# Kernel optimization log

Measured on AMD Instinct MI355X. Metric: run time of the kernel, lower is better.

The kernel has to match this reference:

```python
import jax, jax.numpy as jnp
import numpy as np

BN_EPS = 1e-5


def _l2norm(v, eps=1e-12):
    return v / (jnp.linalg.norm(v) + eps)


def _sn_weight(W, u):
    # torch spectral_norm, n_power_iterations=1; u, v detached, grad flows via W
    v = _l2norm(W.T @ u)
    u_new = _l2norm(W @ v)
    u_new = jax.lax.stop_gradient(u_new)
    v = jax.lax.stop_gradient(v)
    sigma = u_new @ (W @ v)
    return W / sigma


def setup_inputs() -> dict:
    key = jax.random.key(0)
    ks = jax.random.split(key, 8)
    N, E, nfeat, nhid = 65536, 1048576, 64, 128
    x = jax.random.normal(ks[0], (N, nfeat), dtype=jnp.float32)
    edge_index = jax.random.randint(ks[1], (2, E), 0, N, dtype=jnp.int64)
    s1 = 1.0 / np.sqrt(nfeat)
    s2 = 1.0 / np.sqrt(nhid)
    W1 = jax.random.uniform(ks[2], (nhid, nfeat), jnp.float32, -s1, s1)
    b1 = jax.random.uniform(ks[3], (nhid,), jnp.float32, -s1, s1)
    u1 = jax.random.normal(ks[4], (nhid,), dtype=jnp.float32)
    gamma = jnp.ones((nhid,), jnp.float32)
    beta = jnp.zeros((nhid,), jnp.float32)
    W2 = jax.random.uniform(ks[5], (nhid, nhid), jnp.float32, -s2, s2)
    b2 = jax.random.uniform(ks[6], (nhid,), jnp.float32, -s2, s2)
    u2 = jax.random.normal(ks[7], (nhid,), dtype=jnp.float32)
    return {"x": x, "edge_index": edge_index, "W1": W1, "b1": b1, "u1": u1,
            "gamma": gamma, "beta": beta, "W2": W2, "b2": b2, "u2": u2}


def reference(x, edge_index, W1, b1, u1, gamma, beta, W2, b2, u2):
    N = x.shape[0]
    src, dst = edge_index[0], edge_index[1]
    # GIN neighbor sum aggregation: agg[i] = sum_{(j->i)} x[j]
    agg = jax.ops.segment_sum(x[src], dst, num_segments=N)
    h = x + agg  # (1 + eps) * x + agg, eps = 0
    # MLP: SN-Linear -> ReLU -> BatchNorm1d (training stats) -> SN-Linear
    h = h @ _sn_weight(W1, u1).T + b1
    h = jax.nn.relu(h)
    mean = jnp.mean(h, axis=0)
    var = jnp.var(h, axis=0)  # biased, as torch BN uses for normalization
    h = (h - mean) * jax.lax.rsqrt(var + BN_EPS) * gamma + beta
    out = h @ _sn_weight(W2, u2).T + b2
    return out
```

## Files before the change

kernel.cpp:

```cpp
#include <hip/hip_runtime.h>


#define BN_EPS 1e-5f
#define NB   512
#define CAP  2816

typedef float f4 __attribute__((ext_vector_type(4)));
typedef short bf8 __attribute__((ext_vector_type(8)));

__device__ inline short f2bf(float f) {
    unsigned u = __float_as_uint(f);
    u = u + 0x7fffu + ((u >> 16) & 1u);
    return (short)(u >> 16);
}
__device__ inline float bf2f(unsigned short u) {
    return __uint_as_float((unsigned)u << 16);
}
__device__ inline unsigned pk2(float a, float b) {
    return (unsigned)(unsigned short)f2bf(a) |
           ((unsigned)(unsigned short)f2bf(b) << 16);
}

__global__ __launch_bounds__(512) void k1_bin(const int* __restrict__ ei, int E,
                                              int* __restrict__ gcount,
                                              unsigned* __restrict__ pairs,
                                              const float* __restrict__ x,
                                              unsigned* __restrict__ xbf2,
                                              const float* __restrict__ W1,
                                              short* __restrict__ w1bf,
                                              const float* __restrict__ u1,
                                              const float* __restrict__ W2,
                                              const float* __restrict__ u2,
                                              float* __restrict__ sinv) {
    __shared__ int hist[512];
    __shared__ int sbase[512];
    __shared__ int cur[512];
    __shared__ int gofs[512];
    __shared__ unsigned stage[4096];
    int t = threadIdx.x;
    int bid = blockIdx.x;

    if (bid < 256) {
        hist[t] = 0;
        __syncthreads();

        const uint4* s4 = (const uint4*)ei + bid * 1024;
        const uint4* d4 = (const uint4*)(ei + E) + bid * 1024;
        unsigned pk[8];
#pragma unroll
        for (int i = 0; i < 2; i++) {
            int idx = i * 512 + t;
            uint4 sv = s4[idx];
            uint4 dv = d4[idx];
            pk[i * 4 + 0] = ((dv.x >> 7) << 23) | (sv.x << 7) | (dv.x & 127u);
            pk[i * 4 + 1] = ((dv.y >> 7) << 23) | (sv.y << 7) | (dv.y & 127u);
            pk[i * 4 + 2] = ((dv.z >> 7) << 23) | (sv.z << 7) | (dv.z & 127u);
            pk[i * 4 + 3] = ((dv.w >> 7) << 23) | (sv.w << 7) | (dv.w & 127u);
            atomicAdd(&hist[dv.x >> 7], 1);
            atomicAdd(&hist[dv.y >> 7], 1);
            atomicAdd(&hist[dv.z >> 7], 1);
            atomicAdd(&hist[dv.w >> 7], 1);
        }
        __syncthreads();

        int cntb = hist[t];
        for (int o = 1; o < 512; o <<= 1) {
            int v = (t >= o) ? hist[t - o] : 0;
            __syncthreads();
            hist[t] += v;
            __syncthreads();
        }
        int excl = hist[t] - cntb;
        sbase[t] = excl;
        cur[t] = excl;
        __syncthreads();

#pragma unroll
        for (int i = 0; i < 8; i++) {
            int p = atomicAdd(&cur[pk[i] >> 23], 1);
            stage[p] = pk[i];
        }
        __syncthreads();

        gofs[t] = atomicAdd(&gcount[t], cntb);
        __syncthreads();

#pragma unroll
        for (int i = 0; i < 8; i++) {
            int p = i * 512 + t;
            unsigned v = stage[p];
            int b = (int)(v >> 23);
            int li = p - sbase[b];
            pairs[(size_t)b * CAP + gofs[b] + li] = v & 0x7FFFFFu;
        }
    } else if (bid < 512) {
        int cb = bid - 256;
        const float4* xp = (const float4*)x;
#pragma unroll
        for (int k = 0; k < 4; k++) {
            int i = cb * 2048 + k * 512 + t;
            float4 a = xp[2 * i], b = xp[2 * i + 1];
            uint4 o = {pk2(a.x, a.y), pk2(a.z, a.w), pk2(b.x, b.y), pk2(b.z, b.w)};
            ((uint4*)xbf2)[i] = o;
        }
    } else {
#pragma unroll
        for (int k = 0; k < 2; k++) {
            int idx = k * 512 + t;
            const float4* wp = (const float4*)W1;
            float4 a = wp[2 * idx], b = wp[2 * idx + 1];
            uint4 o = {pk2(a.x, a.y), pk2(a.z, a.w), pk2(b.x, b.y), pk2(b.z, b.w)};
            ((uint4*)w1bf)[idx] = o;
        }
        float* red = (float*)stage;
        float* v   = (float*)hist;
        float* sq  = (float*)sbase;

        {
            int j = t & 63, q = t >> 6;
            float s = 0.f;
            for (int i = q * 16; i < q * 16 + 16; i++) s += W1[i * 64 + j] * u1[i];
            red[t] = s;
        }
        __syncthreads();
        if (t < 64) {
            float vj = 0.f;
#pragma unroll
            for (int g = 0; g < 8; g++) vj += red[g * 64 + t];
            v[t] = vj; sq[t] = vj * vj;
        }
        __syncthreads();
        for (int s2 = 32; s2 > 0; s2 >>= 1) {
            if (t < s2) sq[t] += sq[t + s2];
            __syncthreads();
        }
        if (t < 64) v[t] = v[t] / (sqrtf(sq[0]) + 1e-12f);
        __syncthreads();
        {
            int r = t >> 2, h = t & 3;
            const float4* wr = (const float4*)(W1 + r * 64 + h * 16);
            const float4* vv = (const float4*)v + h * 4;
            float s = 0.f;
#pragma unroll
            for (int k = 0; k < 4; k++) {
                float4 a = wr[k]; float4 b = vv[k];
                s += a.x * b.x + a.y * b.y + a.z * b.z + a.w * b.w;
            }
            red[t] = s;
        }
        __syncthreads();
        if (t < 128) {
            float tr = (red[4 * t] + red[4 * t + 1]) + (red[4 * t + 2] + red[4 * t + 3]);
            sq[t] = tr * tr;
        }
        __syncthreads();
        for (int s2 = 64; s2 > 0; s2 >>= 1) {
            if (t < s2) sq[t] += sq[t + s2];
            __syncthreads();
        }
        if (t == 0) { float nt2 = sq[0]; sinv[0] = (sqrtf(nt2) + 1e-12f) / nt2; }
        __syncthreads();

        {
            int j = t & 127, q = t >> 7;
            float s = 0.f;
            for (int i = q * 32; i < q * 32 + 32; i++) s += W2[i * 128 + j] * u2[i];
            red[t] = s;
        }
        __syncthreads();
        if (t < 128) {
            float vj = (red[t] + red[128 + t]) + (red[256 + t] + red[384 + t]);
            v[t] = vj; sq[t] = vj * vj;
        }
        __syncthreads();
        for (int s2 = 64; s2 > 0; s2 >>= 1) {
            if (t < s2) sq[t] += sq[t + s2];
            __syncthreads();
        }
        if (t < 128) v[t] = v[t] / (sqrtf(sq[0]) + 1e-12f);
        __syncthreads();
        {
            int r = t >> 2, h = t & 3;
            const float4* wr = (const float4*)(W2 + r * 128 + h * 32);
            const float4* vv = (const float4*)v + h * 8;
            float s = 0.f;
#pragma unroll
            for (int k = 0; k < 8; k++) {
                float4 a = wr[k]; float4 b = vv[k];
                s += a.x * b.x + a.y * b.y + a.z * b.z + a.w * b.w;
            }
            red[t] = s;
        }
        __syncthreads();
        if (t < 128) {
            float tr = (red[4 * t] + red[4 * t + 1]) + (red[4 * t + 2] + red[4 * t + 3]);
            sq[t] = tr * tr;
        }
        __syncthreads();
        for (int s2 = 64; s2 > 0; s2 >>= 1) {
            if (t < s2) sq[t] += sq[t + s2];
            __syncthreads();
        }
        if (t == 0) { float nt2 = sq[0]; sinv[1] = (sqrtf(nt2) + 1e-12f) / nt2; }
    }
}

__global__ __launch_bounds__(512) void k2_agg_gemm1(
        const unsigned* __restrict__ pairs,
        const int* __restrict__ gcount,
        const unsigned* __restrict__ xbf2,
        const short* __restrict__ w1bf,
        const float* __restrict__ b1,
        const float* __restrict__ sinv,
        char* __restrict__ outbase,
        float* __restrict__ bnacc) {
    __shared__ short u[16384];
    __shared__ unsigned short sorted[CAP];
    __shared__ int hist[128];
    __shared__ int offs[128];
    __shared__ int cur[128];
    __shared__ float red1[1024], red2[1024];
    int t = threadIdx.x;
    int b = blockIdx.x;
    int cnt = gcount[b];

    unsigned* ep = (unsigned*)u;
    {
        const uint4* gp4 = (const uint4*)(pairs + (size_t)b * CAP);
        int cnt4 = (cnt + 3) >> 2;
        for (int j = t; j < cnt4; j += 512) ((uint4*)ep)[j] = gp4[j];
    }
    if (t < 128) hist[t] = 0;
    __syncthreads();
    for (int j = t; j < cnt; j += 512) atomicAdd(&hist[ep[j] & 127u], 1);
    __syncthreads();
    int cntb = (t < 128) ? hist[t] : 0;
    for (int o = 1; o < 128; o <<= 1) {
        int v = (t < 128 && t >= o) ? hist[t - o] : 0;
        __syncthreads();
        if (t < 128) hist[t] += v;
        __syncthreads();
    }
    if (t < 128) { offs[t] = hist[t] - cntb; cur[t] = hist[t] - cntb; }
    __syncthreads();
    for (int j = t; j < cnt; j += 512) {
        unsigned v = ep[j];
        int p = atomicAdd(&cur[v & 127u], 1);
        sorted[p] = (unsigned short)(v >> 7);
    }
    __syncthreads();

    int w = t >> 6;
    int lane = t & 63;
    int h = lane >> 5;
    int l = lane & 31;
    float hr0[16], hr1[16];

#pragma unroll
    for (int ni = 0; ni < 16; ni++) {
        int n = w * 16 + ni;
        int g = b * 128 + n;
        int beg = offs[n], end = hist[n];
        float a0 = 0.f, a1 = 0.f, b0 = 0.f, b1r = 0.f;
        float c0 = 0.f, c1 = 0.f, d0 = 0.f, d1 = 0.f;
        int j = beg + h;
        for (; j + 6 < end; j += 8) {
            int s0 = sorted[j];
            int s1 = sorted[j + 2];
            int s2 = sorted[j + 4];
            int s3 = sorted[j + 6];
            unsigned v0 = xbf2[(size_t)s0 * 32 + l];
            unsigned v1 = xbf2[(size_t)s1 * 32 + l];
            unsigned v2 = xbf2[(size_t)s2 * 32 + l];
            unsigned v3 = xbf2[(size_t)s3 * 32 + l];
            a0 += bf2f((unsigned short)v0); a1 += bf2f((unsigned short)(v0 >> 16));
            b0 += bf2f((unsigned short)v1); b1r += bf2f((unsigned short)(v1 >> 16));
            c0 += bf2f((unsigned short)v2); c1 += bf2f((unsigned short)(v2 >> 16));
            d0 += bf2f((unsigned short)v3); d1 += bf2f((unsigned short)(v3 >> 16));
        }
        for (; j < end; j += 2) {
            unsigned v = xbf2[(size_t)sorted[j] * 32 + l];
            a0 += bf2f((unsigned short)v); a1 += bf2f((unsigned short)(v >> 16));
        }
        a0 = (a0 + b0) + (c0 + d0);
        a1 = (a1 + b1r) + (c1 + d1);
        a0 += __shfl_xor(a0, 32);
        a1 += __shfl_xor(a1, 32);
        unsigned xs = xbf2[(size_t)g * 32 + l];
        a0 += bf2f((unsigned short)xs);
        a1 += bf2f((unsigned short)(xs >> 16));
        hr0[ni] = a0; hr1[ni] = a1;
    }
    __syncthreads();

    if (h == 0) {
#pragma unroll
        for (int ni = 0; ni < 16; ni++) {
            int n = w * 16 + ni;
            int c = l >> 2;
            int cs = c ^ (n & 7);
            *(unsigned*)&u[n * 64 + cs * 8 + (l & 3) * 2] = pk2(hr0[ni], hr1[ni]);
        }
    }
    {
        const bf8* wsrc = (const bf8*)w1bf;
#pragma unroll
        for (int i = 0; i < 2; i++) {
            int idx = i * 512 + t;
            int row = idx >> 3, c = idx & 7;
            int cs = c ^ (row & 7);
            *(bf8*)&u[8192 + row * 64 + cs * 8] = wsrc[idx];
        }
    }
    __syncthreads();

    int l15 = lane & 15, quad = lane >> 4;
    f4 acc[8];
#pragma unroll
    for (int nt = 0; nt < 8; nt++) acc[nt] = (f4){0.f, 0.f, 0.f, 0.f};

#pragma unroll
    for (int ks = 0; ks < 2; ks++) {
        bf8 a, bfr[8];
        {
            int node = w * 16 + l15;
            int cs = (ks * 4 + quad) ^ (node & 7);
            a = *(const bf8*)&u[node * 64 + cs * 8];
        }
#pragma unroll
        for (int nt = 0; nt < 8; nt++) {
            int o = nt * 16 + l15;
            int cs = (ks * 4 + quad) ^ (o & 7);
            bfr[nt] = *(const bf8*)&u[8192 + o * 64 + cs * 8];
        }
#pragma unroll
        for (int nt = 0; nt < 8; nt++)
            acc[nt] = __builtin_amdgcn_mfma_f32_16x16x32_bf16(a, bfr[nt], acc[nt], 0, 0, 0);
    }

    float s1 = sinv[0];
#pragma unroll
    for (int nt = 0; nt < 8; nt++) {
        float bb = b1[nt * 16 + l15];
        float s = 0.f, q = 0.f;
#pragma unroll
        for (int r = 0; r < 4; r++) {
            float v = fmaxf(fmaf(acc[nt][r], s1, bb), 0.f);
            acc[nt][r] = v;
            s += v; q += v * v;
        }
        s += __shfl_xor(s, 16); s += __shfl_xor(s, 32);
        q += __shfl_xor(q, 16); q += __shfl_xor(q, 32);
        if (quad == 0) {
            red1[w * 128 + nt * 16 + l15] = s;
            red2[w * 128 + nt * 16 + l15] = q;
        }
    }
    __syncthreads();

#pragma unroll
    for (int nt = 0; nt < 8; nt++) {
        int col = nt * 16 + l15;
#pragma unroll
        for (int r = 0; r < 4; r++) {
            int row = w * 16 + quad * 4 + r;
            int cs = (col >> 3) ^ (row & 15);
            u[row * 128 + cs * 8 + (col & 7)] = f2bf(acc[nt][r]);
        }
    }
    __syncthreads();

    bf8* dst = (bf8*)(outbase + (size_t)b * 65536);
#pragma unroll
    for (int i = 0; i < 4; i++) {
        int idx = i * 512 + t;
        int row = idx >> 4, c = idx & 15;
        int cs = c ^ (row & 15);
        dst[idx] = *(const bf8*)&u[row * 128 + cs * 8];
    }
    if (t < 128) {
        float s = 0.f, q = 0.f;
#pragma unroll
        for (int g = 0; g < 8; g++) { s += red1[g * 128 + t]; q += red2[g * 128 + t]; }
        atomicAdd(&bnacc[t], s);
        atomicAdd(&bnacc[128 + t], q);
    }
}

__global__ __launch_bounds__(256) void k3_fold_gemm2(
        const float* __restrict__ bnacc, int N,
        const float* __restrict__ gamma,
        const float* __restrict__ beta,
        const float* __restrict__ W2,
        const float* __restrict__ b2,
        const float* __restrict__ sinv,
        char* __restrict__ outbase) {
    __shared__ short s5[32768];
    float* fs = (float*)s5;
    int t = threadIdx.x;
    int b = blockIdx.x;

    if (t < 128) {
        float mean = bnacc[t] / (float)N;
        float var = bnacc[t + 128] / (float)N - mean * mean;
        float rstd = rsqrtf(var + BN_EPS);
        float a = rstd * gamma[t];
        fs[t] = a;
        fs[128 + t] = beta[t] - mean * a;
    }
    __syncthreads();

    float s2 = sinv[1];
    {
        int o = t >> 1;
        int jbase = (t & 1) * 64;
        const float4* wr = (const float4*)(W2 + o * 128 + jbase);
#pragma unroll
        for (int k = 0; k < 8; k++) {
            int c = (jbase >> 3) + k;
            float4 a = wr[2 * k], bb = wr[2 * k + 1];
            int j0 = jbase + k * 8;
            bf8 v;
            v[0] = f2bf(a.x * s2 * fs[j0 + 0]);
            v[1] = f2bf(a.y * s2 * fs[j0 + 1]);
            v[2] = f2bf(a.z * s2 * fs[j0 + 2]);
            v[3] = f2bf(a.w * s2 * fs[j0 + 3]);
            v[4] = f2bf(bb.x * s2 * fs[j0 + 4]);
            v[5] = f2bf(bb.y * s2 * fs[j0 + 5]);
            v[6] = f2bf(bb.z * s2 * fs[j0 + 6]);
            v[7] = f2bf(bb.w * s2 * fs[j0 + 7]);
            int cs = c ^ (o & 15);
            *(bf8*)&s5[16384 + o * 128 + cs * 8] = v;
        }
    }
    if (t < 128) {
        float accb = 0.f;
        for (int j = 0; j < 128; j++)
            accb += W2[t * 128 + j] * s2 * fs[128 + j];
        fs[256 + t] = b2[t] + accb;
    }
    __syncthreads();

    int w = t >> 6;
    int lane = t & 63;
    int l15 = lane & 15, quad = lane >> 4;
    float b2v[8];
#pragma unroll
    for (int nt = 0; nt < 8; nt++) b2v[nt] = fs[256 + nt * 16 + l15];
    __syncthreads();

    {
        const bf8* hsrc = (const bf8*)(outbase + (size_t)b * 65536);
#pragma unroll
        for (int i = 0; i < 8; i++) {
            int idx = i * 256 + t;
            int row = idx >> 4, c = idx & 15;
            int cs = c ^ (row & 15);
            *(bf8*)&s5[row * 128 + cs * 8] = hsrc[idx];
        }
    }
    __syncthreads();

    f4 acc[2][8];
#pragma unroll
    for (int mt = 0; mt < 2; mt++)
#pragma unroll
        for (int nt = 0; nt < 8; nt++) acc[mt][nt] = (f4){0.f, 0.f, 0.f, 0.f};

#pragma unroll
    for (int ks = 0; ks < 4; ks++) {
        bf8 a[2], bfr[8];
#pragma unroll
        for (int mt = 0; mt < 2; mt++) {
            int node = w * 32 + mt * 16 + l15;
            int cs = (ks * 4 + quad) ^ (node & 15);
            a[mt] = *(const bf8*)&s5[node * 128 + cs * 8];
        }
#pragma unroll
        for (int nt = 0; nt < 8; nt++) {
            int o = nt * 16 + l15;
            int cs = (ks * 4 + quad) ^ (o & 15);
            bfr[nt] = *(const bf8*)&s5[16384 + o * 128 + cs * 8];
        }
#pragma unroll
        for (int mt = 0; mt < 2; mt++)
#pragma unroll
            for (int nt = 0; nt < 8; nt++)
                acc[mt][nt] = __builtin_amdgcn_mfma_f32_16x16x32_bf16(
                    a[mt], bfr[nt], acc[mt][nt], 0, 0, 0);
    }

    float* out = (float*)(outbase + (size_t)b * 65536);
#pragma unroll
    for (int mt = 0; mt < 2; mt++)
#pragma unroll
        for (int nt = 0; nt < 8; nt++)
#pragma unroll
            for (int r = 0; r < 4; r++) {
                int row = w * 32 + mt * 16 + quad * 4 + r;
                out[(size_t)row * 128 + nt * 16 + l15] = acc[mt][nt][r] + b2v[nt];
            }
}

extern "C" void kernel_launch(void* const* d_in, const int* in_sizes, int n_in,
                              void* d_out, int out_size, void* d_ws, size_t ws_size,
                              hipStream_t stream) {
    const float* x     = (const float*)d_in[0];
    const int*   ei    = (const int*)d_in[1];
    const float* W1    = (const float*)d_in[2];
    const float* b1    = (const float*)d_in[3];
    const float* u1    = (const float*)d_in[4];
    const float* gamma = (const float*)d_in[5];
    const float* beta  = (const float*)d_in[6];
    const float* W2    = (const float*)d_in[7];
    const float* b2    = (const float*)d_in[8];
    const float* u2    = (const float*)d_in[9];

    int N = in_sizes[0] / 64;
    int E = in_sizes[1] / 2;

    char* ws = (char*)d_ws;
    size_t off = 0;
    unsigned* pairs = (unsigned*)(ws + off); off += (size_t)NB * CAP * 4;
    unsigned short* xbf = (unsigned short*)(ws + off); off += (size_t)N * 64 * 2;
    int*   gcount  = (int*)(ws + off);   off += 512 * 4;
    float* bnacc   = (float*)(ws + off); off += 256 * 4;
    float* sinv    = (float*)(ws + off); off += 16 * 4;
    short* w1bf    = (short*)(ws + off); off += 128 * 64 * 2;

    hipMemsetAsync(gcount, 0, 512 * 4 + 256 * 4, stream);
    k1_bin<<<513, 512, 0, stream>>>(ei, E, gcount, pairs, x, (unsigned*)xbf,
                                    W1, w1bf, u1, W2, u2, sinv);
    k2_agg_gemm1<<<NB, 512, 0, stream>>>(pairs, gcount, (const unsigned*)xbf,
                                         w1bf, b1, sinv, (char*)d_out, bnacc);
    k3_fold_gemm2<<<NB, 256, 0, stream>>>(bnacc, N, gamma, beta, W2, b2, sinv,
                                          (char*)d_out);
}
```

Measured before the change: 164.3 us.

## Interleave gather of two nodes, predicate tails, overlap W1 staging, raise occupancy

```diff
diff --git a/kernel.cpp b/kernel.cpp
--- a/kernel.cpp
+++ b/kernel.cpp
@@ -205,7 +205,7 @@
     }
 }
 
-__global__ __launch_bounds__(512) void k2_agg_gemm1(
+__global__ __launch_bounds__(512, 4) void k2_agg_gemm1(
         const unsigned* __restrict__ pairs,
         const int* __restrict__ gcount,
         const unsigned* __restrict__ xbf2,
@@ -250,58 +250,6 @@
     }
     __syncthreads();
 
-    int w = t >> 6;
-    int lane = t & 63;
-    int h = lane >> 5;
-    int l = lane & 31;
-    float hr0[16], hr1[16];
-
-#pragma unroll
-    for (int ni = 0; ni < 16; ni++) {
-        int n = w * 16 + ni;
-        int g = b * 128 + n;
-        int beg = offs[n], end = hist[n];
-        float a0 = 0.f, a1 = 0.f, b0 = 0.f, b1r = 0.f;
-        float c0 = 0.f, c1 = 0.f, d0 = 0.f, d1 = 0.f;
-        int j = beg + h;
-        for (; j + 6 < end; j += 8) {
-            int s0 = sorted[j];
-            int s1 = sorted[j + 2];
-            int s2 = sorted[j + 4];
-            int s3 = sorted[j + 6];
-            unsigned v0 = xbf2[(size_t)s0 * 32 + l];
-            unsigned v1 = xbf2[(size_t)s1 * 32 + l];
-            unsigned v2 = xbf2[(size_t)s2 * 32 + l];
-            unsigned v3 = xbf2[(size_t)s3 * 32 + l];
-            a0 += bf2f((unsigned short)v0); a1 += bf2f((unsigned short)(v0 >> 16));
-            b0 += bf2f((unsigned short)v1); b1r += bf2f((unsigned short)(v1 >> 16));
-            c0 += bf2f((unsigned short)v2); c1 += bf2f((unsigned short)(v2 >> 16));
-            d0 += bf2f((unsigned short)v3); d1 += bf2f((unsigned short)(v3 >> 16));
-        }
-        for (; j < end; j += 2) {
-            unsigned v = xbf2[(size_t)sorted[j] * 32 + l];
-            a0 += bf2f((unsigned short)v); a1 += bf2f((unsigned short)(v >> 16));
-        }
-        a0 = (a0 + b0) + (c0 + d0);
-        a1 = (a1 + b1r) + (c1 + d1);
-        a0 += __shfl_xor(a0, 32);
-        a1 += __shfl_xor(a1, 32);
-        unsigned xs = xbf2[(size_t)g * 32 + l];
-        a0 += bf2f((unsigned short)xs);
-        a1 += bf2f((unsigned short)(xs >> 16));
-        hr0[ni] = a0; hr1[ni] = a1;
-    }
-    __syncthreads();
-
-    if (h == 0) {
-#pragma unroll
-        for (int ni = 0; ni < 16; ni++) {
-            int n = w * 16 + ni;
-            int c = l >> 2;
-            int cs = c ^ (n & 7);
-            *(unsigned*)&u[n * 64 + cs * 8 + (l & 3) * 2] = pk2(hr0[ni], hr1[ni]);
-        }
-    }
     {
         const bf8* wsrc = (const bf8*)w1bf;
 #pragma unroll
@@ -310,6 +258,120 @@
             int row = idx >> 3, c = idx & 7;
             int cs = c ^ (row & 7);
             *(bf8*)&u[8192 + row * 64 + cs * 8] = wsrc[idx];
+        }
+    }
+
+    int w = t >> 6;
+    int lane = t & 63;
+    int h = lane >> 5;
+    int l = lane & 31;
+
+#pragma unroll
+    for (int np = 0; np < 8; np++) {
+        int nA = w * 16 + np * 2;
+        int nB = nA + 1;
+        unsigned xsA = xbf2[(size_t)(b * 128 + nA) * 32 + l];
+        unsigned xsB = xbf2[(size_t)(b * 128 + nB) * 32 + l];
+        int begA = offs[nA], endA = hist[nA];
+        int begB = offs[nB], endB = hist[nB];
+        float aA0 = 0.f, aA1 = 0.f, bA0 = 0.f, bA1 = 0.f;
+        float cA0 = 0.f, cA1 = 0.f, dA0 = 0.f, dA1 = 0.f;
+        float aB0 = 0.f, aB1 = 0.f, bB0 = 0.f, bB1 = 0.f;
+        float cB0 = 0.f, cB1 = 0.f, dB0 = 0.f, dB1 = 0.f;
+        int jA = begA + h, jB = begB + h;
+        while (jA + 6 < endA && jB + 6 < endB) {
+            int sA0 = sorted[jA],     sA1 = sorted[jA + 2];
+            int sA2 = sorted[jA + 4], sA3 = sorted[jA + 6];
+            int sB0 = sorted[jB],     sB1 = sorted[jB + 2];
+            int sB2 = sorted[jB + 4], sB3 = sorted[jB + 6];
+            unsigned vA0 = xbf2[(size_t)sA0 * 32 + l];
+            unsigned vA1 = xbf2[(size_t)sA1 * 32 + l];
+            unsigned vA2 = xbf2[(size_t)sA2 * 32 + l];
+            unsigned vA3 = xbf2[(size_t)sA3 * 32 + l];
+            unsigned vB0 = xbf2[(size_t)sB0 * 32 + l];
+            unsigned vB1 = xbf2[(size_t)sB1 * 32 + l];
+            unsigned vB2 = xbf2[(size_t)sB2 * 32 + l];
+            unsigned vB3 = xbf2[(size_t)sB3 * 32 + l];
+            aA0 += bf2f((unsigned short)vA0); aA1 += bf2f((unsigned short)(vA0 >> 16));
+            bA0 += bf2f((unsigned short)vA1); bA1 += bf2f((unsigned short)(vA1 >> 16));
+            cA0 += bf2f((unsigned short)vA2); cA1 += bf2f((unsigned short)(vA2 >> 16));
+            dA0 += bf2f((unsigned short)vA3); dA1 += bf2f((unsigned short)(vA3 >> 16));
+            aB0 += bf2f((unsigned short)vB0); aB1 += bf2f((unsigned short)(vB0 >> 16));
+            bB0 += bf2f((unsigned short)vB1); bB1 += bf2f((unsigned short)(vB1 >> 16));
+            cB0 += bf2f((unsigned short)vB2); cB1 += bf2f((unsigned short)(vB2 >> 16));
+            dB0 += bf2f((unsigned short)vB3); dB1 += bf2f((unsigned short)(vB3 >> 16));
+            jA += 8; jB += 8;
+        }
+        while (jA + 6 < endA) {
+            int s0 = sorted[jA],     s1 = sorted[jA + 2];
+            int s2 = sorted[jA + 4], s3 = sorted[jA + 6];
+            unsigned v0 = xbf2[(size_t)s0 * 32 + l];
+            unsigned v1 = xbf2[(size_t)s1 * 32 + l];
+            unsigned v2 = xbf2[(size_t)s2 * 32 + l];
+            unsigned v3 = xbf2[(size_t)s3 * 32 + l];
+            aA0 += bf2f((unsigned short)v0); aA1 += bf2f((unsigned short)(v0 >> 16));
+            bA0 += bf2f((unsigned short)v1); bA1 += bf2f((unsigned short)(v1 >> 16));
+            cA0 += bf2f((unsigned short)v2); cA1 += bf2f((unsigned short)(v2 >> 16));
+            dA0 += bf2f((unsigned short)v3); dA1 += bf2f((unsigned short)(v3 >> 16));
+            jA += 8;
+        }
+        while (jB + 6 < endB) {
+            int s0 = sorted[jB],     s1 = sorted[jB + 2];
+            int s2 = sorted[jB + 4], s3 = sorted[jB + 6];
+            unsigned v0 = xbf2[(size_t)s0 * 32 + l];
+            unsigned v1 = xbf2[(size_t)s1 * 32 + l];
+            unsigned v2 = xbf2[(size_t)s2 * 32 + l];
+            unsigned v3 = xbf2[(size_t)s3 * 32 + l];
+            aB0 += bf2f((unsigned short)v0); aB1 += bf2f((unsigned short)(v0 >> 16));
+            bB0 += bf2f((unsigned short)v1); bB1 += bf2f((unsigned short)(v1 >> 16));
+            cB0 += bf2f((unsigned short)v2); cB1 += bf2f((unsigned short)(v2 >> 16));
+            dB0 += bf2f((unsigned short)v3); dB1 += bf2f((unsigned short)(v3 >> 16));
+            jB += 8;
+        }
+        {
+            bool pA0 = jA < endA, pA1 = jA + 2 < endA, pA2 = jA + 4 < endA;
+            bool pB0 = jB < endB, pB1 = jB + 2 < endB, pB2 = jB + 4 < endB;
+            int iA0 = pA0 ? jA : 0, iA1 = pA1 ? jA + 2 : 0, iA2 = pA2 ? jA + 4 : 0;
+            int iB0 = pB0 ? jB : 0, iB1 = pB1 ? jB + 2 : 0, iB2 = pB2 ? jB + 4 : 0;
+            int sA0 = sorted[iA0], sA1 = sorted[iA1], sA2 = sorted[iA2];
+            int sB0 = sorted[iB0], sB1 = sorted[iB1], sB2 = sorted[iB2];
+            unsigned vA0 = xbf2[(size_t)sA0 * 32 + l];
+            unsigned vA1 = xbf2[(size_t)sA1 * 32 + l];
+            unsigned vA2 = xbf2[(size_t)sA2 * 32 + l];
+            unsigned vB0 = xbf2[(size_t)sB0 * 32 + l];
+            unsigned vB1 = xbf2[(size_t)sB1 * 32 + l];
+            unsigned vB2 = xbf2[(size_t)sB2 * 32 + l];
+            aA0 += pA0 ? bf2f((unsigned short)vA0) : 0.f;
+            aA1 += pA0 ? bf2f((unsigned short)(vA0 >> 16)) : 0.f;
+            bA0 += pA1 ? bf2f((unsigned short)vA1) : 0.f;
+            bA1 += pA1 ? bf2f((unsigned short)(vA1 >> 16)) : 0.f;
+            cA0 += pA2 ? bf2f((unsigned short)vA2) : 0.f;
+            cA1 += pA2 ? bf2f((unsigned short)(vA2 >> 16)) : 0.f;
+            aB0 += pB0 ? bf2f((unsigned short)vB0) : 0.f;
+            aB1 += pB0 ? bf2f((unsigned short)(vB0 >> 16)) : 0.f;
+            bB0 += pB1 ? bf2f((unsigned short)vB1) : 0.f;
+            bB1 += pB1 ? bf2f((unsigned short)(vB1 >> 16)) : 0.f;
+            cB0 += pB2 ? bf2f((unsigned short)vB2) : 0.f;
+            cB1 += pB2 ? bf2f((unsigned short)(vB2 >> 16)) : 0.f;
+        }
+        float sA0f = (aA0 + bA0) + (cA0 + dA0);
+        float sA1f = (aA1 + bA1) + (cA1 + dA1);
+        float sB0f = (aB0 + bB0) + (cB0 + dB0);
+        float sB1f = (aB1 + bB1) + (cB1 + dB1);
+        sA0f += __shfl_xor(sA0f, 32);
+        sA1f += __shfl_xor(sA1f, 32);
+        sB0f += __shfl_xor(sB0f, 32);
+        sB1f += __shfl_xor(sB1f, 32);
+        sA0f += bf2f((unsigned short)xsA);
+        sA1f += bf2f((unsigned short)(xsA >> 16));
+        sB0f += bf2f((unsigned short)xsB);
+        sB1f += bf2f((unsigned short)(xsB >> 16));
+        if (h == 0) {
+            int c = l >> 2;
+            int csA = c ^ (nA & 7);
+            int csB = c ^ (nB & 7);
+            *(unsigned*)&u[nA * 64 + csA * 8 + (l & 3) * 2] = pk2(sA0f, sA1f);
+            *(unsigned*)&u[nB * 64 + csB * 8 + (l & 3) * 2] = pk2(sB0f, sB1f);
         }
     }
     __syncthreads();
@@ -434,10 +496,15 @@
         }
     }
     if (t < 128) {
+        const float4* wr = (const float4*)(W2 + t * 128);
         float accb = 0.f;
-        for (int j = 0; j < 128; j++)
-            accb += W2[t * 128 + j] * s2 * fs[128 + j];
-        fs[256 + t] = b2[t] + accb;
+#pragma unroll
+        for (int k = 0; k < 32; k++) {
+            float4 a = wr[k];
+            accb += a.x * fs[128 + 4 * k + 0] + a.y * fs[128 + 4 * k + 1] +
+                    a.z * fs[128 + 4 * k + 2] + a.w * fs[128 + 4 * k + 3];
+        }
+        fs[256 + t] = b2[t] + accb * s2;
     }
     __syncthreads();
 
```

After: 155.7 us. 1.06x faster.

## Gather neighbor rows with 16-byte loads, two nodes per wave interleaved

Applied to the files above, without the earlier changes.

```diff
diff --git a/kernel.cpp b/kernel.cpp
--- a/kernel.cpp
+++ b/kernel.cpp
@@ -19,6 +19,22 @@
 __device__ inline unsigned pk2(float a, float b) {
     return (unsigned)(unsigned short)f2bf(a) |
            ((unsigned)(unsigned short)f2bf(b) << 16);
+}
+__device__ inline void acc8(float* f, uint4 v) {
+    f[0] += bf2f((unsigned short)v.x); f[1] += bf2f((unsigned short)(v.x >> 16));
+    f[2] += bf2f((unsigned short)v.y); f[3] += bf2f((unsigned short)(v.y >> 16));
+    f[4] += bf2f((unsigned short)v.z); f[5] += bf2f((unsigned short)(v.z >> 16));
+    f[6] += bf2f((unsigned short)v.w); f[7] += bf2f((unsigned short)(v.w >> 16));
+}
+__device__ inline void acc8p(float* f, uint4 v, bool p) {
+    f[0] += p ? bf2f((unsigned short)v.x) : 0.f;
+    f[1] += p ? bf2f((unsigned short)(v.x >> 16)) : 0.f;
+    f[2] += p ? bf2f((unsigned short)v.y) : 0.f;
+    f[3] += p ? bf2f((unsigned short)(v.y >> 16)) : 0.f;
+    f[4] += p ? bf2f((unsigned short)v.z) : 0.f;
+    f[5] += p ? bf2f((unsigned short)(v.z >> 16)) : 0.f;
+    f[6] += p ? bf2f((unsigned short)v.w) : 0.f;
+    f[7] += p ? bf2f((unsigned short)(v.w >> 16)) : 0.f;
 }
 
 __global__ __launch_bounds__(512) void k1_bin(const int* __restrict__ ei, int E,
@@ -205,7 +221,7 @@
     }
 }
 
-__global__ __launch_bounds__(512) void k2_agg_gemm1(
+__global__ __launch_bounds__(512, 4) void k2_agg_gemm1(
         const unsigned* __restrict__ pairs,
         const int* __restrict__ gcount,
         const unsigned* __restrict__ xbf2,
@@ -250,58 +266,6 @@
     }
     __syncthreads();
 
-    int w = t >> 6;
-    int lane = t & 63;
-    int h = lane >> 5;
-    int l = lane & 31;
-    float hr0[16], hr1[16];
-
-#pragma unroll
-    for (int ni = 0; ni < 16; ni++) {
-        int n = w * 16 + ni;
-        int g = b * 128 + n;
-        int beg = offs[n], end = hist[n];
-        float a0 = 0.f, a1 = 0.f, b0 = 0.f, b1r = 0.f;
-        float c0 = 0.f, c1 = 0.f, d0 = 0.f, d1 = 0.f;
-        int j = beg + h;
-        for (; j + 6 < end; j += 8) {
-            int s0 = sorted[j];
-            int s1 = sorted[j + 2];
-            int s2 = sorted[j + 4];
-            int s3 = sorted[j + 6];
-            unsigned v0 = xbf2[(size_t)s0 * 32 + l];
-            unsigned v1 = xbf2[(size_t)s1 * 32 + l];
-            unsigned v2 = xbf2[(size_t)s2 * 32 + l];
-            unsigned v3 = xbf2[(size_t)s3 * 32 + l];
-            a0 += bf2f((unsigned short)v0); a1 += bf2f((unsigned short)(v0 >> 16));
-            b0 += bf2f((unsigned short)v1); b1r += bf2f((unsigned short)(v1 >> 16));
-            c0 += bf2f((unsigned short)v2); c1 += bf2f((unsigned short)(v2 >> 16));
-            d0 += bf2f((unsigned short)v3); d1 += bf2f((unsigned short)(v3 >> 16));
-        }
-        for (; j < end; j += 2) {
-            unsigned v = xbf2[(size_t)sorted[j] * 32 + l];
-            a0 += bf2f((unsigned short)v); a1 += bf2f((unsigned short)(v >> 16));
-        }
-        a0 = (a0 + b0) + (c0 + d0);
-        a1 = (a1 + b1r) + (c1 + d1);
-        a0 += __shfl_xor(a0, 32);
-        a1 += __shfl_xor(a1, 32);
-        unsigned xs = xbf2[(size_t)g * 32 + l];
-        a0 += bf2f((unsigned short)xs);
-        a1 += bf2f((unsigned short)(xs >> 16));
-        hr0[ni] = a0; hr1[ni] = a1;
-    }
-    __syncthreads();
-
-    if (h == 0) {
-#pragma unroll
-        for (int ni = 0; ni < 16; ni++) {
-            int n = w * 16 + ni;
-            int c = l >> 2;
-            int cs = c ^ (n & 7);
-            *(unsigned*)&u[n * 64 + cs * 8 + (l & 3) * 2] = pk2(hr0[ni], hr1[ni]);
-        }
-    }
     {
         const bf8* wsrc = (const bf8*)w1bf;
 #pragma unroll
@@ -310,6 +274,83 @@
             int row = idx >> 3, c = idx & 7;
             int cs = c ^ (row & 7);
             *(bf8*)&u[8192 + row * 64 + cs * 8] = wsrc[idx];
+        }
+    }
+
+    int w = t >> 6;
+    int lane = t & 63;
+    int l7 = lane & 7;
+    int oct = lane >> 3;
+    const uint4* xb4 = (const uint4*)xbf2;
+
+#pragma unroll
+    for (int np = 0; np < 8; np++) {
+        int nA = w * 16 + np * 2;
+        int nB = nA + 1;
+        uint4 xsA = xb4[(size_t)(b * 128 + nA) * 8 + l7];
+        uint4 xsB = xb4[(size_t)(b * 128 + nB) * 8 + l7];
+        int bA = offs[nA], eA = hist[nA];
+        int bB = offs[nB], eB = hist[nB];
+        float fA[8] = {0.f, 0.f, 0.f, 0.f, 0.f, 0.f, 0.f, 0.f};
+        float fB[8] = {0.f, 0.f, 0.f, 0.f, 0.f, 0.f, 0.f, 0.f};
+        while (bA + 7 < eA && bB + 7 < eB) {
+            int sA = sorted[bA + oct];
+            int sB = sorted[bB + oct];
+            uint4 vA = xb4[(size_t)sA * 8 + l7];
+            uint4 vB = xb4[(size_t)sB * 8 + l7];
+            acc8(fA, vA);
+            acc8(fB, vB);
+            bA += 8; bB += 8;
+        }
+        while (bA + 7 < eA) {
+            int sA = sorted[bA + oct];
+            uint4 vA = xb4[(size_t)sA * 8 + l7];
+            acc8(fA, vA);
+            bA += 8;
+        }
+        while (bB + 7 < eB) {
+            int sB = sorted[bB + oct];
+            uint4 vB = xb4[(size_t)sB * 8 + l7];
+            acc8(fB, vB);
+            bB += 8;
+        }
+        {
+            bool pA = bA + oct < eA;
+            bool pB = bB + oct < eB;
+            int iA = pA ? bA + oct : 0;
+            int iB = pB ? bB + oct : 0;
+            int sA = sorted[iA];
+            int sB = sorted[iB];
+            uint4 vA = xb4[(size_t)sA * 8 + l7];
+            uint4 vB = xb4[(size_t)sB * 8 + l7];
+            acc8p(fA, vA, pA);
+            acc8p(fB, vB, pB);
+        }
+#pragma unroll
+        for (int i = 0; i < 8; i++) {
+            fA[i] += __shfl_xor(fA[i], 8);
+            fA[i] += __shfl_xor(fA[i], 16);
+            fA[i] += __shfl_xor(fA[i], 32);
+            fB[i] += __shfl_xor(fB[i], 8);
+            fB[i] += __shfl_xor(fB[i], 16);
+            fB[i] += __shfl_xor(fB[i], 32);
+        }
+        if (oct == 0) {
+            fA[0] += bf2f((unsigned short)xsA.x); fA[1] += bf2f((unsigned short)(xsA.x >> 16));
+            fA[2] += bf2f((unsigned short)xsA.y); fA[3] += bf2f((unsigned short)(xsA.y >> 16));
+            fA[4] += bf2f((unsigned short)xsA.z); fA[5] += bf2f((unsigned short)(xsA.z >> 16));
+            fA[6] += bf2f((unsigned short)xsA.w); fA[7] += bf2f((unsigned short)(xsA.w >> 16));
+            fB[0] += bf2f((unsigned short)xsB.x); fB[1] += bf2f((unsigned short)(xsB.x >> 16));
+            fB[2] += bf2f((unsigned short)xsB.y); fB[3] += bf2f((unsigned short)(xsB.y >> 16));
+            fB[4] += bf2f((unsigned short)xsB.z); fB[5] += bf2f((unsigned short)(xsB.z >> 16));
+            fB[6] += bf2f((unsigned short)xsB.w); fB[7] += bf2f((unsigned short)(xsB.w >> 16));
+            bf8 hA, hB;
+#pragma unroll
+            for (int i = 0; i < 8; i++) { hA[i] = f2bf(fA[i]); hB[i] = f2bf(fB[i]); }
+            int csA = l7 ^ (nA & 7);
+            int csB = l7 ^ (nB & 7);
+            *(bf8*)&u[nA * 64 + csA * 8] = hA;
+            *(bf8*)&u[nB * 64 + csB * 8] = hB;
         }
     }
     __syncthreads();
@@ -434,10 +475,15 @@
         }
     }
     if (t < 128) {
+        const float4* wr = (const float4*)(W2 + t * 128);
         float accb = 0.f;
-        for (int j = 0; j < 128; j++)
-            accb += W2[t * 128 + j] * s2 * fs[128 + j];
-        fs[256 + t] = b2[t] + accb;
+#pragma unroll
+        for (int k = 0; k < 32; k++) {
+            float4 a = wr[k];
+            accb += a.x * fs[128 + 4 * k + 0] + a.y * fs[128 + 4 * k + 1] +
+                    a.z * fs[128 + 4 * k + 2] + a.w * fs[128 + 4 * k + 3];
+        }
+        fs[256 + t] = b2[t] + accb * s2;
     }
     __syncthreads();
 
```

After: 162.8 us. About the same (-0.9%).

## Replace per-bin sort with LDS float atomics and widen aggregation block

Applied to the files above, without the earlier changes.

```diff
diff --git a/kernel.cpp b/kernel.cpp
--- a/kernel.cpp
+++ b/kernel.cpp
@@ -63,16 +63,24 @@
         }
         __syncthreads();
 
-        int cntb = hist[t];
-        for (int o = 1; o < 512; o <<= 1) {
-            int v = (t >= o) ? hist[t - o] : 0;
-            __syncthreads();
-            hist[t] += v;
-            __syncthreads();
-        }
-        int excl = hist[t] - cntb;
-        sbase[t] = excl;
-        cur[t] = excl;
+        if (t < 64) {
+            int e[8]; int s = 0;
+#pragma unroll
+            for (int k = 0; k < 8; k++) { e[k] = hist[8 * t + k]; s += e[k]; }
+#pragma unroll
+            for (int o = 1; o < 64; o <<= 1) {
+                int v = __shfl_up(s, o);
+                if (t >= o) s += v;
+            }
+            int run = s;
+#pragma unroll
+            for (int k = 7; k >= 0; k--) {
+                hist[8 * t + k] = run;
+                run -= e[k];
+                sbase[8 * t + k] = run;
+                cur[8 * t + k] = run;
+            }
+        }
         __syncthreads();
 
 #pragma unroll
@@ -82,6 +90,7 @@
         }
         __syncthreads();
 
+        int cntb = hist[t] - sbase[t];
         gofs[t] = atomicAdd(&gcount[t], cntb);
         __syncthreads();
 
@@ -205,7 +214,7 @@
     }
 }
 
-__global__ __launch_bounds__(512) void k2_agg_gemm1(
+__global__ __launch_bounds__(1024, 8) void k2_agg_gemm1(
         const unsigned* __restrict__ pairs,
         const int* __restrict__ gcount,
         const unsigned* __restrict__ xbf2,
@@ -214,169 +223,135 @@
         const float* __restrict__ sinv,
         char* __restrict__ outbase,
         float* __restrict__ bnacc) {
-    __shared__ short u[16384];
-    __shared__ unsigned short sorted[CAP];
-    __shared__ int hist[128];
-    __shared__ int offs[128];
-    __shared__ int cur[128];
+    __shared__ float hf[8192];
+    __shared__ short w1s[8192];
     __shared__ float red1[1024], red2[1024];
     int t = threadIdx.x;
     int b = blockIdx.x;
     int cnt = gcount[b];
 
-    unsigned* ep = (unsigned*)u;
     {
-        const uint4* gp4 = (const uint4*)(pairs + (size_t)b * CAP);
-        int cnt4 = (cnt + 3) >> 2;
-        for (int j = t; j < cnt4; j += 512) ((uint4*)ep)[j] = gp4[j];
-    }
-    if (t < 128) hist[t] = 0;
-    __syncthreads();
-    for (int j = t; j < cnt; j += 512) atomicAdd(&hist[ep[j] & 127u], 1);
-    __syncthreads();
-    int cntb = (t < 128) ? hist[t] : 0;
-    for (int o = 1; o < 128; o <<= 1) {
-        int v = (t < 128 && t >= o) ? hist[t - o] : 0;
-        __syncthreads();
-        if (t < 128) hist[t] += v;
-        __syncthreads();
-    }
-    if (t < 128) { offs[t] = hist[t] - cntb; cur[t] = hist[t] - cntb; }
-    __syncthreads();
-    for (int j = t; j < cnt; j += 512) {
-        unsigned v = ep[j];
-        int p = atomicAdd(&cur[v & 127u], 1);
-        sorted[p] = (unsigned short)(v >> 7);
+        float4* z4 = (float4*)hf;
+#pragma unroll
+        for (int i = 0; i < 2; i++) z4[i * 1024 + t] = (float4){0.f, 0.f, 0.f, 0.f};
+    }
+    {
+        const bf8* wsrc = (const bf8*)w1bf;
+        int row = t >> 3, c = t & 7;
+        int cs = c ^ (row & 7);
+        *(bf8*)&w1s[row * 64 + cs * 8] = wsrc[t];
     }
     __syncthreads();
 
     int w = t >> 6;
     int lane = t & 63;
-    int h = lane >> 5;
+    int hl = lane >> 5;
     int l = lane & 31;
-    float hr0[16], hr1[16];
-
-#pragma unroll
-    for (int ni = 0; ni < 16; ni++) {
-        int n = w * 16 + ni;
-        int g = b * 128 + n;
-        int beg = offs[n], end = hist[n];
-        float a0 = 0.f, a1 = 0.f, b0 = 0.f, b1r = 0.f;
-        float c0 = 0.f, c1 = 0.f, d0 = 0.f, d1 = 0.f;
-        int j = beg + h;
-        for (; j + 6 < end; j += 8) {
-            int s0 = sorted[j];
-            int s1 = sorted[j + 2];
-            int s2 = sorted[j + 4];
-            int s3 = sorted[j + 6];
-            unsigned v0 = xbf2[(size_t)s0 * 32 + l];
-            unsigned v1 = xbf2[(size_t)s1 * 32 + l];
-            unsigned v2 = xbf2[(size_t)s2 * 32 + l];
-            unsigned v3 = xbf2[(size_t)s3 * 32 + l];
-            a0 += bf2f((unsigned short)v0); a1 += bf2f((unsigned short)(v0 >> 16));
-            b0 += bf2f((unsigned short)v1); b1r += bf2f((unsigned short)(v1 >> 16));
-            c0 += bf2f((unsigned short)v2); c1 += bf2f((unsigned short)(v2 >> 16));
-            d0 += bf2f((unsigned short)v3); d1 += bf2f((unsigned short)(v3 >> 16));
-        }
-        for (; j < end; j += 2) {
-            unsigned v = xbf2[(size_t)sorted[j] * 32 + l];
-            a0 += bf2f((unsigned short)v); a1 += bf2f((unsigned short)(v >> 16));
-        }
-        a0 = (a0 + b0) + (c0 + d0);
-        a1 = (a1 + b1r) + (c1 + d1);
-        a0 += __shfl_xor(a0, 32);
-        a1 += __shfl_xor(a1, 32);
-        unsigned xs = xbf2[(size_t)g * 32 + l];
-        a0 += bf2f((unsigned short)xs);
-        a1 += bf2f((unsigned short)(xs >> 16));
-        hr0[ni] = a0; hr1[ni] = a1;
-    }
-    __syncthreads();
-
-    if (h == 0) {
-#pragma unroll
-        for (int ni = 0; ni < 16; ni++) {
-            int n = w * 16 + ni;
-            int c = l >> 2;
-            int cs = c ^ (n & 7);
-            *(unsigned*)&u[n * 64 + cs * 8 + (l & 3) * 2] = pk2(hr0[ni], hr1[ni]);
-        }
-    }
-    {
-        const bf8* wsrc = (const bf8*)w1bf;
-#pragma unroll
-        for (int i = 0; i < 2; i++) {
-            int idx = i * 512 + t;
-            int row = idx >> 3, c = idx & 7;
-            int cs = c ^ (row & 7);
-            *(bf8*)&u[8192 + row * 64 + cs * 8] = wsrc[idx];
-        }
+    const unsigned* pg = pairs + (size_t)b * CAP;
+
+    int npairs = (cnt + 1) >> 1;
+    for (int jp = w * 4; jp < npairs; jp += 64) {
+#pragma unroll
+        for (int k = 0; k < 4; k++) {
+            int e = 2 * (jp + k) + hl;
+            bool p = e < cnt;
+            unsigned pv = pg[p ? e : 0];
+            int src = (int)(pv >> 7);
+            int d = (int)(pv & 127u);
+            unsigned xv = xbf2[(size_t)src * 32 + l];
+            float f0 = p ? bf2f((unsigned short)xv) : 0.f;
+            float f1 = p ? bf2f((unsigned short)(xv >> 16)) : 0.f;
+            int base = d * 64 + (((l >> 2) ^ (d & 7)) << 3) + 2 * (l & 3);
+            atomicAdd(&hf[base], f0);
+            atomicAdd(&hf[base + 1], f1);
+        }
+    }
+    __syncthreads();
+
+#pragma unroll
+    for (int i = 0; i < 4; i++) {
+        int idx = i * 1024 + t;
+        int n = idx >> 5, ll = idx & 31;
+        unsigned xv = xbf2[(size_t)(b * 128 + n) * 32 + ll];
+        int base = n * 64 + (((ll >> 2) ^ (n & 7)) << 3) + 2 * (ll & 3);
+        hf[base]     += bf2f((unsigned short)xv);
+        hf[base + 1] += bf2f((unsigned short)(xv >> 16));
     }
     __syncthreads();
 
     int l15 = lane & 15, quad = lane >> 4;
+    float s1 = sinv[0];
     f4 acc[8];
 #pragma unroll
     for (int nt = 0; nt < 8; nt++) acc[nt] = (f4){0.f, 0.f, 0.f, 0.f};
 
-#pragma unroll
-    for (int ks = 0; ks < 2; ks++) {
-        bf8 a, bfr[8];
-        {
-            int node = w * 16 + l15;
-            int cs = (ks * 4 + quad) ^ (node & 7);
-            a = *(const bf8*)&u[node * 64 + cs * 8];
-        }
+    if (t < 512) {
+#pragma unroll
+        for (int ks = 0; ks < 2; ks++) {
+            bf8 a, bfr[8];
+            {
+                int node = w * 16 + l15;
+                int cs = (ks * 4 + quad) ^ (node & 7);
+                const float4* ap = (const float4*)&hf[node * 64 + cs * 8];
+                float4 a0 = ap[0], a1 = ap[1];
+                a[0] = f2bf(a0.x); a[1] = f2bf(a0.y);
+                a[2] = f2bf(a0.z); a[3] = f2bf(a0.w);
+                a[4] = f2bf(a1.x); a[5] = f2bf(a1.y);
+                a[6] = f2bf(a1.z); a[7] = f2bf(a1.w);
+            }
+#pragma unroll
+            for (int nt = 0; nt < 8; nt++) {
+                int o = nt * 16 + l15;
+                int cs = (ks * 4 + quad) ^ (o & 7);
+                bfr[nt] = *(const bf8*)&w1s[o * 64 + cs * 8];
+            }
+#pragma unroll
+            for (int nt = 0; nt < 8; nt++)
+                acc[nt] = __builtin_amdgcn_mfma_f32_16x16x32_bf16(a, bfr[nt], acc[nt], 0, 0, 0);
+        }
+
 #pragma unroll
         for (int nt = 0; nt < 8; nt++) {
-            int o = nt * 16 + l15;
-            int cs = (ks * 4 + quad) ^ (o & 7);
-            bfr[nt] = *(const bf8*)&u[8192 + o * 64 + cs * 8];
-        }
-#pragma unroll
-        for (int nt = 0; nt < 8; nt++)
-            acc[nt] = __builtin_amdgcn_mfma_f32_16x16x32_bf16(a, bfr[nt], acc[nt], 0, 0, 0);
-    }
-
-    float s1 = sinv[0];
-#pragma unroll
-    for (int nt = 0; nt < 8; nt++) {
-        float bb = b1[nt * 16 + l15];
-        float s = 0.f, q = 0.f;
-#pragma unroll
-        for (int r = 0; r < 4; r++) {
-            float v = fmaxf(fmaf(acc[nt][r], s1, bb), 0.f);
-            acc[nt][r] = v;
-            s += v; q += v * v;
-        }
-        s += __shfl_xor(s, 16); s += __shfl_xor(s, 32);
-        q += __shfl_xor(q, 16); q += __shfl_xor(q, 32);
-        if (quad == 0) {
-            red1[w * 128 + nt * 16 + l15] = s;
-            red2[w * 128 + nt * 16 + l15] = q;
-        }
-    }
-    __syncthreads();
-
-#pragma unroll
-    for (int nt = 0; nt < 8; nt++) {
-        int col = nt * 16 + l15;
-#pragma unroll
-        for (int r = 0; r < 4; r++) {
-            int row = w * 16 + quad * 4 + r;
-            int cs = (col >> 3) ^ (row & 15);
-            u[row * 128 + cs * 8 + (col & 7)] = f2bf(acc[nt][r]);
+            float bb = b1[nt * 16 + l15];
+            float s = 0.f, q = 0.f;
+#pragma unroll
+            for (int r = 0; r < 4; r++) {
+                float v = fmaxf(fmaf(acc[nt][r], s1, bb), 0.f);
+                acc[nt][r] = v;
+                s += v; q += v * v;
+            }
+            s += __shfl_xor(s, 16); s += __shfl_xor(s, 32);
+            q += __shfl_xor(q, 16); q += __shfl_xor(q, 32);
+            if (quad == 0) {
+                red1[w * 128 + nt * 16 + l15] = s;
+                red2[w * 128 + nt * 16 + l15] = q;
+            }
+        }
+    }
+    __syncthreads();
+
+    short* u16 = (short*)hf;
+    if (t < 512) {
+#pragma unroll
+        for (int nt = 0; nt < 8; nt++) {
+            int col = nt * 16 + l15;
+#pragma unroll
+            for (int r = 0; r < 4; r++) {
+                int row = w * 16 + quad * 4 + r;
+                int cs = (col >> 3) ^ (row & 15);
+                u16[row * 128 + cs * 8 + (col & 7)] = f2bf(acc[nt][r]);
+            }
         }
     }
     __syncthreads();
 
     bf8* dst = (bf8*)(outbase + (size_t)b * 65536);
 #pragma unroll
-    for (int i = 0; i < 4; i++) {
-        int idx = i * 512 + t;
+    for (int i = 0; i < 2; i++) {
+        int idx = i * 1024 + t;
         int row = idx >> 4, c = idx & 15;
         int cs = c ^ (row & 15);
-        dst[idx] = *(const bf8*)&u[row * 128 + cs * 8];
+        dst[idx] = *(const bf8*)&u16[row * 128 + cs * 8];
     }
     if (t < 128) {
         float s = 0.f, q = 0.f;
@@ -434,10 +409,15 @@
         }
     }
     if (t < 128) {
+        const float4* wr = (const float4*)(W2 + t * 128);
         float accb = 0.f;
-        for (int j = 0; j < 128; j++)
-            accb += W2[t * 128 + j] * s2 * fs[128 + j];
-        fs[256 + t] = b2[t] + accb;
+#pragma unroll
+        for (int k = 0; k < 32; k++) {
+            float4 a = wr[k];
+            accb += a.x * fs[128 + 4 * k + 0] + a.y * fs[128 + 4 * k + 1] +
+                    a.z * fs[128 + 4 * k + 2] + a.w * fs[128 + 4 * k + 3];
+        }
+        fs[256 + t] = b2[t] + accb * s2;
     }
     __syncthreads();
 
@@ -531,8 +511,8 @@
     hipMemsetAsync(gcount, 0, 512 * 4 + 256 * 4, stream);
     k1_bin<<<513, 512, 0, stream>>>(ei, E, gcount, pairs, x, (unsigned*)xbf,
                                     W1, w1bf, u1, W2, u2, sinv);
-    k2_agg_gemm1<<<NB, 512, 0, stream>>>(pairs, gcount, (const unsigned*)xbf,
-                                         w1bf, b1, sinv, (char*)d_out, bnacc);
+    k2_agg_gemm1<<<NB, 1024, 0, stream>>>(pairs, gcount, (const unsigned*)xbf,
+                                          w1bf, b1, sinv, (char*)d_out, bnacc);
     k3_fold_gemm2<<<NB, 256, 0, stream>>>(bnacc, N, gamma, beta, W2, b2, sinv,
                                           (char*)d_out);
 }
```

Result: slower. 476.4 us (+189.9%).
